# Performance work log

Measured on AMD Instinct MI355X. Metric: run time of the kernel, lower is better.

## Reference

```python
import jax, jax.numpy as jnp
import numpy as np

BATCH, SEQ, H, P, N, L = 8, 8192, 16, 64, 64, 64  # batch, seq, heads, d_head, d_state, block_len


def setup_inputs() -> dict:
    key = jax.random.key(0)
    k1, k2, k3 = jax.random.split(key, 3)
    X = jax.random.normal(k1, (BATCH, SEQ, H, P), dtype=jnp.float32)
    # A is the log-decay; scale down so exp(cumsum) stays finite over 8192 steps
    A = jax.random.normal(k2, (BATCH, SEQ, H), dtype=jnp.float32) * 0.02
    B = jax.random.normal(k3, (BATCH, SEQ, H, N), dtype=jnp.float32)
    return {"X": X, "A": A, "B": B}


def reference(X, A, B):
    b, s, h, p = X.shape
    n = B.shape[-1]
    l = L
    c = s // l  # n_chunks

    Xb = X.reshape(b, c, l, h, p)                      # (b,c,l,h,p)
    Ab = A.reshape(b, c, l, h).transpose(0, 3, 1, 2)   # (b,h,c,l)
    Bb = B.reshape(b, c, l, h, n)                      # (b,c,l,h,n)

    # intra-chunk cumulative decay
    A_cs = jnp.cumsum(Ab, axis=-1)                     # (b,h,c,l)
    decay_states = jnp.exp(A_cs[..., -1:] - A_cs)      # (b,h,c,l)

    # per-chunk state: sum_l decay * B outer X -> (b,c,h,p,n)
    states = jnp.einsum('bhcl,bclhn,bclhp->bchpn', decay_states, Bb, Xb)

    # prepend zero initial state
    init = jnp.zeros((b, 1, h, p, n), dtype=X.dtype)
    all_states = jnp.concatenate([init, states], axis=1)  # (b,c+1,h,p,n)

    # cross-chunk decay-weighted combination into final state
    A_ends = A_cs[..., -1]                                # (b,h,c)
    A_pad_cs = jnp.cumsum(jnp.pad(A_ends, ((0, 0), (0, 0), (1, 0))), axis=-1)  # (b,h,c+1)
    decay_chunk = jnp.exp(A_pad_cs[..., -1:] - A_pad_cs)  # (b,h,c+1)

    final_states = jnp.einsum('bhc,bchpn->bhpn', decay_chunk, all_states)  # (b,h,p,n)
    return final_states
```

## Files before the change

### kernel.cpp

```cpp
#include <hip/hip_runtime.h>

#define BATCH 8
#define SEQ   8192
#define NH    16
#define DP    64
#define ROWF  (NH*DP)
#define HGRP  4
#define NTHR  512
#define KT    32
#define RS    257

typedef __attribute__((ext_vector_type(8))) short bf16x8;
typedef __attribute__((ext_vector_type(4))) float f32x4;

static __device__ __forceinline__ unsigned pk2(float lo, float hi) {
    unsigned a = __builtin_bit_cast(unsigned, lo);
    unsigned b = __builtin_bit_cast(unsigned, hi);
    a = (a + 0x7FFFu + ((a >> 16) & 1u)) >> 16;
    b = (b + 0x7FFFu + ((b >> 16) & 1u)) & 0xFFFF0000u;
    return (a & 0xFFFFu) | b;
}

template<int NBLK>
__global__ __launch_bounds__(NTHR)
void k_partial(const float* __restrict__ Xg, const float* __restrict__ Ag,
               const float* __restrict__ Bg, float* __restrict__ part,
               float* __restrict__ blockA)
{
    constexpr int TB  = SEQ / NBLK;
    constexpr int Q   = TB / 64;
    constexpr int NKT = TB / KT;

    __shared__ unsigned XL[16][RS];
    __shared__ unsigned BL[16][RS];
    __shared__ float    WT[HGRP][TB];

    const int gid  = blockIdx.x;
    const int blk  = gid % NBLK;
    const int hg   = (gid / NBLK) & 3;
    const int b    = gid / (4 * NBLK);
    const int tid  = threadIdx.x;
    const int w    = tid >> 6;
    const int lane = tid & 63;
    const int hloc = w >> 1;
    const int nh   = w & 1;
    const int h    = hg * HGRP + hloc;
    const int t0   = blk * TB;

    float c[Q];
    {
        const size_t abase = ((size_t)(b * SEQ + t0 + lane * Q)) * NH + h;
        float run = 0.f;
        #pragma unroll
        for (int k = 0; k < Q; ++k) { run += Ag[abase + (size_t)k * NH]; c[k] = run; }
    }
    float tsum = c[Q - 1], s = tsum;
    #pragma unroll
    for (int d = 1; d < 64; d <<= 1) {
        float o = __shfl_up(s, d, 64);
        if (lane >= d) s += o;
    }
    const float total = __shfl(s, 63, 64);
    const float excl  = s - tsum;
    if (nh == 0) {
        #pragma unroll
        for (int k = 0; k < Q; ++k)
            WT[hloc][lane * Q + k] = __expf(total - (excl + c[k]));
        if (lane == 63) blockA[(size_t)(b * NH + h) * NBLK + blk] = total;
    }

    f32x4 acc[4][2];
    #pragma unroll
    for (int mi = 0; mi < 4; ++mi)
        #pragma unroll
        for (int ni = 0; ni < 2; ++ni) acc[mi][ni] = (f32x4){0.f, 0.f, 0.f, 0.f};

    const int hl = lane >> 4;
    const int p4 = (lane & 15) * 4;
    const size_t gbase = (size_t)(b * SEQ + t0) * ROWF + hg * (HGRP * DP) + hl * DP + p4;

    auto issue = [&](int k, float4* lx, float4* lb) {
        if (k >= NKT) return;
        const size_t tb = gbase + (size_t)(k * KT + w * 4) * ROWF;
        #pragma unroll
        for (int i = 0; i < 4; ++i) {
            lx[i] = *(const float4*)(Xg + tb + (size_t)i * ROWF);
            lb[i] = *(const float4*)(Bg + tb + (size_t)i * ROWF);
        }
    };
    auto cwrite = [&](int k, const float4* lx, const float4* lb) {
        const int tIn = k * KT + w * 4;
        #pragma unroll
        for (int q = 0; q < 2; ++q) {
            const float w0 = WT[hl][tIn + 2 * q];
            const float w1 = WT[hl][tIn + 2 * q + 1];
            const int   tp = w * 2 + q;
            const float* x0 = (const float*)&lx[2 * q];
            const float* x1 = (const float*)&lx[2 * q + 1];
            const float* b0 = (const float*)&lb[2 * q];
            const float* b1 = (const float*)&lb[2 * q + 1];
            #pragma unroll
            for (int pp = 0; pp < 4; ++pp) {
                XL[tp][hl * 64 + p4 + pp] = pk2(x0[pp] * w0, x1[pp] * w1);
                BL[tp][hl * 64 + p4 + pp] = pk2(b0[pp], b1[pp]);
            }
        }
    };
    auto compute = [&]() {
        const int r  = lane & 15;
        const int kg = lane >> 4;
        uint4 af[4], bf[2];
        #pragma unroll
        for (int mi = 0; mi < 4; ++mi) {
            const int row = hloc * 64 + mi * 16 + r;
            af[mi].x = XL[kg * 4 + 0][row];
            af[mi].y = XL[kg * 4 + 1][row];
            af[mi].z = XL[kg * 4 + 2][row];
            af[mi].w = XL[kg * 4 + 3][row];
        }
        #pragma unroll
        for (int ni = 0; ni < 2; ++ni) {
            const int row = hloc * 64 + nh * 32 + ni * 16 + r;
            bf[ni].x = BL[kg * 4 + 0][row];
            bf[ni].y = BL[kg * 4 + 1][row];
            bf[ni].z = BL[kg * 4 + 2][row];
            bf[ni].w = BL[kg * 4 + 3][row];
        }
        #pragma unroll
        for (int mi = 0; mi < 4; ++mi) {
            const bf16x8 a = __builtin_bit_cast(bf16x8, af[mi]);
            #pragma unroll
            for (int ni = 0; ni < 2; ++ni) {
                const bf16x8 bb = __builtin_bit_cast(bf16x8, bf[ni]);
                acc[mi][ni] = __builtin_amdgcn_mfma_f32_16x16x32_bf16(
                                  a, bb, acc[mi][ni], 0, 0, 0);
            }
        }
    };

    float4 sx0[4], sb0[4], sx1[4], sb1[4];
    issue(0, sx0, sb0);
    issue(1, sx1, sb1);
    __syncthreads();

    #pragma unroll 1
    for (int k = 0; k < NKT; k += 2) {
        cwrite(k, sx0, sb0);
        issue(k + 2, sx0, sb0);
        asm volatile("s_waitcnt lgkmcnt(0)" ::: "memory");
        __builtin_amdgcn_s_barrier();
        __builtin_amdgcn_sched_barrier(0);
        compute();
        __builtin_amdgcn_s_barrier();

        cwrite(k + 1, sx1, sb1);
        issue(k + 3, sx1, sb1);
        asm volatile("s_waitcnt lgkmcnt(0)" ::: "memory");
        __builtin_amdgcn_s_barrier();
        __builtin_amdgcn_sched_barrier(0);
        compute();
        __builtin_amdgcn_s_barrier();
    }

    float* dst = part + ((size_t)(b * NH + h) * NBLK + blk) * 4096;
    {
        const int r  = lane & 15;
        const int cg = lane >> 4;
        #pragma unroll
        for (int mi = 0; mi < 4; ++mi)
            #pragma unroll
            for (int ni = 0; ni < 2; ++ni)
                #pragma unroll
                for (int rr = 0; rr < 4; ++rr)
                    dst[(mi * 16 + cg * 4 + rr) * 64 + nh * 32 + ni * 16 + r] =
                        acc[mi][ni][rr];
    }
}

__global__ void k_scales(const float* __restrict__ blockA, float* __restrict__ scale,
                         int nblk)
{
    const int bh = blockIdx.x * blockDim.x + threadIdx.x;
    if (bh < BATCH * NH) {
        float run = 0.f;
        for (int c2 = nblk - 1; c2 >= 0; --c2) {
            scale[bh * nblk + c2] = __expf(run);
            run += blockA[bh * nblk + c2];
        }
    }
}

__global__ __launch_bounds__(256)
void k_combine(const float* __restrict__ part, const float* __restrict__ scale,
               float* __restrict__ out, int nblk)
{
    const int idx = blockIdx.x * 256 + threadIdx.x;
    const int bh  = idx >> 12;
    const int e   = idx & 4095;
    float r = 0.f;
    for (int q = 0; q < nblk; ++q)
        r += scale[bh * nblk + q] * part[((size_t)bh * nblk + q) * 4096 + e];
    out[idx] = r;
}

extern "C" void kernel_launch(void* const* d_in, const int* in_sizes, int n_in,
                              void* d_out, int out_size, void* d_ws, size_t ws_size,
                              hipStream_t stream)
{
    const float* X = (const float*)d_in[0];
    const float* A = (const float*)d_in[1];
    const float* B = (const float*)d_in[2];
    float* out     = (float*)d_out;

    const size_t need32 = ((size_t)BATCH * NH * 32 * 4096 + 2ull * BATCH * NH * 32) * 4;
    const int nblk = (ws_size >= need32) ? 32 : 16;

    float* part   = (float*)d_ws;
    float* blockA = part + (size_t)BATCH * NH * nblk * 4096;
    float* scale  = blockA + (size_t)BATCH * NH * nblk;

    if (nblk == 32)
        hipLaunchKernelGGL((k_partial<32>), dim3(BATCH * 4 * 32), dim3(NTHR), 0, stream,
                           X, A, B, part, blockA);
    else
        hipLaunchKernelGGL((k_partial<16>), dim3(BATCH * 4 * 16), dim3(NTHR), 0, stream,
                           X, A, B, part, blockA);

    hipLaunchKernelGGL(k_scales, dim3(1), dim3(128), 0, stream, blockA, scale, nblk);
    hipLaunchKernelGGL(k_combine, dim3((BATCH * NH * 4096) / 256), dim3(256), 0, stream,
                       part, scale, out, nblk);
}
```

Baseline: 142.5 us.

## Fuse scale computation into combine, vectorize LDS writes, remap blocks per XCD

Drops the separate single-block k_scales launch: k_combine now computes the running decay exponentials itself, iterating over blocks in reverse. The cwrite stage packs four bf16 pairs into one 128-bit LDS store instead of scalar stores, with the LDS row stride padded to 260 so those stores stay 16-byte aligned. Block indices are remapped so that consecutive workgroups, which land on different XCDs, cover the same head group and adjacent time blocks, aiming at better L2 locality. The trade-offs are redundant exp work per combine thread and possible LDS bank conflicts in the compute reads at the new stride.

New measurement: 135.7 us. 1.05x faster.

```diff
diff --git a/kernel.cpp b/kernel.cpp
--- a/kernel.cpp
+++ b/kernel.cpp
@@ -8,7 +8,7 @@
 #define HGRP  4
 #define NTHR  512
 #define KT    32
-#define RS    257
+#define RS    260
 
 typedef __attribute__((ext_vector_type(8))) short bf16x8;
 typedef __attribute__((ext_vector_type(4))) float f32x4;
@@ -35,10 +35,15 @@
     __shared__ unsigned BL[16][RS];
     __shared__ float    WT[HGRP][TB];
 
-    const int gid  = blockIdx.x;
-    const int blk  = gid % NBLK;
-    const int hg   = (gid / NBLK) & 3;
-    const int b    = gid / (4 * NBLK);
+    const int p    = blockIdx.x;
+    const int xcd  = p & 7;
+    const int q_   = p >> 3;
+    const int hg   = q_ & 3;
+    const int sidx = q_ >> 2;
+    const int idx  = sidx * 8 + xcd;
+    const int blk  = idx % NBLK;
+    const int b    = idx / NBLK;
+
     const int tid  = threadIdx.x;
     const int w    = tid >> 6;
     const int lane = tid & 63;
@@ -91,19 +96,25 @@
     auto cwrite = [&](int k, const float4* lx, const float4* lb) {
         const int tIn = k * KT + w * 4;
         #pragma unroll
-        for (int q = 0; q < 2; ++q) {
-            const float w0 = WT[hl][tIn + 2 * q];
-            const float w1 = WT[hl][tIn + 2 * q + 1];
-            const int   tp = w * 2 + q;
-            const float* x0 = (const float*)&lx[2 * q];
-            const float* x1 = (const float*)&lx[2 * q + 1];
-            const float* b0 = (const float*)&lb[2 * q];
-            const float* b1 = (const float*)&lb[2 * q + 1];
-            #pragma unroll
-            for (int pp = 0; pp < 4; ++pp) {
-                XL[tp][hl * 64 + p4 + pp] = pk2(x0[pp] * w0, x1[pp] * w1);
-                BL[tp][hl * 64 + p4 + pp] = pk2(b0[pp], b1[pp]);
-            }
+        for (int q2 = 0; q2 < 2; ++q2) {
+            const float w0 = WT[hl][tIn + 2 * q2];
+            const float w1 = WT[hl][tIn + 2 * q2 + 1];
+            const int   tp = w * 2 + q2;
+            const float* x0 = (const float*)&lx[2 * q2];
+            const float* x1 = (const float*)&lx[2 * q2 + 1];
+            const float* b0 = (const float*)&lb[2 * q2];
+            const float* b1 = (const float*)&lb[2 * q2 + 1];
+            uint4 xv, bv;
+            xv.x = pk2(x0[0] * w0, x1[0] * w1);
+            xv.y = pk2(x0[1] * w0, x1[1] * w1);
+            xv.z = pk2(x0[2] * w0, x1[2] * w1);
+            xv.w = pk2(x0[3] * w0, x1[3] * w1);
+            bv.x = pk2(b0[0], b1[0]);
+            bv.y = pk2(b0[1], b1[1]);
+            bv.z = pk2(b0[2], b1[2]);
+            bv.w = pk2(b0[3], b1[3]);
+            *(uint4*)&XL[tp][hl * 64 + p4] = xv;
+            *(uint4*)&BL[tp][hl * 64 + p4] = bv;
         }
     };
     auto compute = [&]() {
@@ -177,29 +188,18 @@
     }
 }
 
-__global__ void k_scales(const float* __restrict__ blockA, float* __restrict__ scale,
-                         int nblk)
-{
-    const int bh = blockIdx.x * blockDim.x + threadIdx.x;
-    if (bh < BATCH * NH) {
-        float run = 0.f;
-        for (int c2 = nblk - 1; c2 >= 0; --c2) {
-            scale[bh * nblk + c2] = __expf(run);
-            run += blockA[bh * nblk + c2];
-        }
-    }
-}
-
 __global__ __launch_bounds__(256)
-void k_combine(const float* __restrict__ part, const float* __restrict__ scale,
+void k_combine(const float* __restrict__ part, const float* __restrict__ blockA,
                float* __restrict__ out, int nblk)
 {
     const int idx = blockIdx.x * 256 + threadIdx.x;
     const int bh  = idx >> 12;
     const int e   = idx & 4095;
-    float r = 0.f;
-    for (int q = 0; q < nblk; ++q)
-        r += scale[bh * nblk + q] * part[((size_t)bh * nblk + q) * 4096 + e];
+    float r = 0.f, run = 0.f;
+    for (int q = nblk - 1; q >= 0; --q) {
+        r   += __expf(run) * part[((size_t)bh * nblk + q) * 4096 + e];
+        run += blockA[bh * nblk + q];
+    }
     out[idx] = r;
 }
 
@@ -212,12 +212,11 @@
     const float* B = (const float*)d_in[2];
     float* out     = (float*)d_out;
 
-    const size_t need32 = ((size_t)BATCH * NH * 32 * 4096 + 2ull * BATCH * NH * 32) * 4;
+    const size_t need32 = ((size_t)BATCH * NH * 32 * 4096 + (size_t)BATCH * NH * 32) * 4;
     const int nblk = (ws_size >= need32) ? 32 : 16;
 
     float* part   = (float*)d_ws;
     float* blockA = part + (size_t)BATCH * NH * nblk * 4096;
-    float* scale  = blockA + (size_t)BATCH * NH * nblk;
 
     if (nblk == 32)
         hipLaunchKernelGGL((k_partial<32>), dim3(BATCH * 4 * 32), dim3(NTHR), 0, stream,
@@ -226,7 +225,6 @@
         hipLaunchKernelGGL((k_partial<16>), dim3(BATCH * 4 * 16), dim3(NTHR), 0, stream,
                            X, A, B, part, blockA);
 
-    hipLaunchKernelGGL(k_scales, dim3(1), dim3(128), 0, stream, blockA, scale, nblk);
     hipLaunchKernelGGL(k_combine, dim3((BATCH * NH * 4096) / 256), dim3(256), 0, stream,
-                       part, scale, out, nblk);
-}
+                       part, blockA, out, nblk);
+}
```
